# Kernel tuning notes

Hardware: AMD Instinct MI355X
Metric: run time of the kernel (lower is better)

Reference implementation:

```python
import jax, jax.numpy as jnp
import numpy as np
import math

D_MODEL = 1024
N_HEADS = 16
N_QUBITS = 8
HEAD_DIM = D_MODEL // N_HEADS
B, L = 2, 2048


def setup_inputs() -> dict:
    key = jax.random.key(0)
    ks = jax.random.split(key, 16)
    s = 0.02
    return {
        "query": jax.random.normal(ks[0], (B, L, D_MODEL), jnp.float32),
        "key_": jax.random.normal(ks[1], (B, L, D_MODEL), jnp.float32),
        "value": jax.random.normal(ks[2], (B, L, D_MODEL), jnp.float32),
        "Wq": jax.random.normal(ks[3], (D_MODEL, D_MODEL), jnp.float32) * s,
        "bq": jnp.zeros((D_MODEL,), jnp.float32),
        "Wk": jax.random.normal(ks[4], (D_MODEL, D_MODEL), jnp.float32) * s,
        "bk": jnp.zeros((D_MODEL,), jnp.float32),
        "Wv": jax.random.normal(ks[5], (D_MODEL, D_MODEL), jnp.float32) * s,
        "bv": jnp.zeros((D_MODEL,), jnp.float32),
        "Wo": jax.random.normal(ks[6], (D_MODEL, D_MODEL), jnp.float32) * s,
        "bo": jnp.zeros((D_MODEL,), jnp.float32),
        "Wf": jax.random.normal(ks[7], (HEAD_DIM, N_QUBITS), jnp.float32) * s,  # feature map weight (input->qubits)
        "bf": jnp.zeros((N_QUBITS,), jnp.float32),
        "quantum_weights": jax.random.normal(ks[8], (N_HEADS, N_QUBITS), jnp.float32) * 0.1,
        "entanglement_strength": jnp.asarray(0.5, jnp.float32),
    }


def _heads(x):
    # [B, L, D] -> [B, H, L, head_dim]
    b, l, _ = x.shape
    return x.reshape(b, l, N_HEADS, HEAD_DIM).transpose(0, 2, 1, 3)


def reference(query, key_, value, Wq, bq, Wk, bk, Wv, bv, Wo, bo, Wf, bf, quantum_weights, entanglement_strength):
    Qh = _heads(query @ Wq.T + bq)   # [B,H,L,d]
    Kh = _heads(key_ @ Wk.T + bk)
    Vh = _heads(value @ Wv.T + bv)

    classical = jnp.einsum("bhid,bhjd->bhij", Qh, Kh) / math.sqrt(HEAD_DIM)

    # quantum feature map: tanh(linear) -> [B,H,L,Q]
    qq = jnp.tanh(jnp.einsum("bhld,dq->bhlq", Qh, Wf) + bf)
    kq = jnp.tanh(jnp.einsum("bhld,dq->bhlq", Kh, Wf) + bf)

    # mean_q w_q*cos(qq_i - kq_j) == (1/Q)[(w*cos qq)@cos(kq)^T + (w*sin qq)@sin(kq)^T]
    w = jax.nn.sigmoid(quantum_weights)[None, :, None, :]  # [1,H,1,Q]
    quantum = (
        jnp.einsum("bhiq,bhjq->bhij", jnp.cos(qq) * w, jnp.cos(kq))
        + jnp.einsum("bhiq,bhjq->bhij", jnp.sin(qq) * w, jnp.sin(kq))
    ) / N_QUBITS
    ent = jax.nn.sigmoid(entanglement_strength)
    quantum = quantum * ent

    mix = ent  # same sigmoid(entanglement_strength) used as mixing weight
    combined = (1.0 - mix) * classical + mix * quantum

    attn = jax.nn.softmax(combined, axis=-1)  # [B,H,L,L]
    attended = jnp.einsum("bhij,bhjd->bhid", attn, Vh)
    attended = attended.transpose(0, 2, 1, 3).reshape(query.shape[0], query.shape[1], D_MODEL)
    output = attended @ Wo.T + bo
    return output, attn.mean(axis=1)
```

## Files before the change

kernel.cpp:

```cpp
#include <hip/hip_runtime.h>


typedef unsigned short u16;
typedef unsigned int u32;
typedef short v8s __attribute__((ext_vector_type(8)));
typedef float v4f __attribute__((ext_vector_type(4)));

static __device__ __forceinline__ float b2f(u16 h) {
  union { u32 u; float f; } a; a.u = ((u32)h) << 16; return a.f;
}
static __device__ __forceinline__ u16 f2b(float f) {
  union { float f; u32 u; } a; a.f = f;
  u32 u = a.u;
  u32 r = u + 0x7FFFu + ((u >> 16) & 1u);
  return (u16)(r >> 16);
}
static __device__ __forceinline__ u32 fbits(float f) {
  union { float f; u32 u; } a; a.f = f; return a.u;
}
static __device__ __forceinline__ v4f mfma16(v8s a, v8s b, v4f c) {
  return __builtin_amdgcn_mfma_f32_16x16x32_bf16(a, b, c, 0, 0, 0);
}
static __device__ __forceinline__ void gload16(const u16* g, u16* l) {
  __builtin_amdgcn_global_load_lds((const __attribute__((address_space(1))) u32*)g,
                                   (__attribute__((address_space(3))) u32*)l, 16, 0, 0);
}

__global__ __launch_bounds__(256) void k_f2b_all(const float* __restrict__ q, const float* __restrict__ k,
                                                 const float* __restrict__ v, const float* __restrict__ wq,
                                                 const float* __restrict__ wk, const float* __restrict__ wv,
                                                 const float* __restrict__ wo, u16* __restrict__ y) {
  int i = blockIdx.x * 256 + threadIdx.x;
  const float* src; int off;
  if (i < 1048576)      { src = q;  off = i; }
  else if (i < 2097152) { src = k;  off = i - 1048576; }
  else if (i < 3145728) { src = v;  off = i - 2097152; }
  else if (i < 3407872) { src = wq; off = i - 3145728; }
  else if (i < 3670016) { src = wk; off = i - 3407872; }
  else if (i < 3932160) { src = wv; off = i - 3670016; }
  else                  { src = wo; off = i - 3932160; }
  float4 val = ((const float4*)src)[off];
  union { u16 s[4]; uint2 u; } o;
  o.s[0] = f2b(val.x); o.s[1] = f2b(val.y); o.s[2] = f2b(val.z); o.s[3] = f2b(val.w);
  ((uint2*)y)[i] = o.u;
}

__global__ __launch_bounds__(256) void k_gemm128(
    const u16* __restrict__ A0, const u16* __restrict__ A1, const u16* __restrict__ A2,
    const u16* __restrict__ B0, const u16* __restrict__ B1, const u16* __restrict__ B2,
    const float* __restrict__ bias0, const float* __restrict__ bias1, const float* __restrict__ bias2,
    u16* __restrict__ O0, u16* __restrict__ O1, u16* __restrict__ O2t,
    float* __restrict__ Cf) {
  __shared__ __align__(16) u16 pool[18432];
  u16* As = pool;
  u16* Bs = pool + 8192;
  const int K = 1024, N = 1024;
  int t = threadIdx.x, w = t >> 6, lane = t & 63, quad = lane >> 4, l16 = lane & 15;
  int z = blockIdx.z;
  const u16* A = (z == 0) ? A0 : (z == 1) ? A1 : A2;
  const u16* Bm = (z == 0) ? B0 : (z == 1) ? B1 : B2;
  const float* bias = (z == 0) ? bias0 : (z == 1) ? bias1 : bias2;
  int n0 = blockIdx.x * 128, m0 = blockIdx.y * 128;

  int srow = lane >> 2, scol = (lane & 3) * 8;
  const u16* gp[8]; u16* lp[8];
#pragma unroll
  for (int qi = 0; qi < 8; ++qi) {
    int mat = qi >> 2, kk = (qi >> 1) & 1, g = w + (qi & 1) * 4;
    int row = g * 16 + srow;
    gp[qi] = (mat ? Bm + (size_t)(n0 + row) * K : A + (size_t)(m0 + row) * K) + kk * 32 + scol;
    lp[qi] = (mat ? Bs : As) + kk * 4096 + g * 512;
  }

  int mrow = (w >> 1) * 64, ncol = (w & 1) * 64;
  v4f zf = {0.f, 0.f, 0.f, 0.f};
  v4f acc[4][4];
#pragma unroll
  for (int mi = 0; mi < 4; ++mi)
#pragma unroll
    for (int ni = 0; ni < 4; ++ni) acc[mi][ni] = zf;

  for (int k0 = 0; k0 < K; k0 += 64) {
    __syncthreads();
#pragma unroll
    for (int qi = 0; qi < 8; ++qi) gload16(gp[qi] + k0, lp[qi]);
    __syncthreads();
#pragma unroll
    for (int kk = 0; kk < 2; ++kk) {
      v8s af[4], bfr[4];
#pragma unroll
      for (int x = 0; x < 4; ++x) {
        af[x] = *(const v8s*)&As[kk * 4096 + (mrow + x * 16 + l16) * 32 + quad * 8];
        bfr[x] = *(const v8s*)&Bs[kk * 4096 + (ncol + x * 16 + l16) * 32 + quad * 8];
      }
#pragma unroll
      for (int mi = 0; mi < 4; ++mi)
#pragma unroll
        for (int ni = 0; ni < 4; ++ni)
          acc[mi][ni] = mfma16(af[mi], bfr[ni], acc[mi][ni]);
    }
  }

  float bv[4];
#pragma unroll
  for (int ni = 0; ni < 4; ++ni) bv[ni] = bias[n0 + ncol + ni * 16 + l16];

  if (Cf) {
#pragma unroll
    for (int mi = 0; mi < 4; ++mi)
#pragma unroll
      for (int ni = 0; ni < 4; ++ni)
#pragma unroll
        for (int r = 0; r < 4; ++r)
          Cf[(size_t)(m0 + mrow + mi * 16 + quad * 4 + r) * N + n0 + ncol + ni * 16 + l16] =
              acc[mi][ni][r] + bv[ni];
  } else if (z != 2) {
    u16* O = z ? O1 : O0;
#pragma unroll
    for (int mi = 0; mi < 4; ++mi)
#pragma unroll
      for (int ni = 0; ni < 4; ++ni)
#pragma unroll
        for (int r = 0; r < 4; ++r)
          O[(size_t)(m0 + mrow + mi * 16 + quad * 4 + r) * N + n0 + ncol + ni * 16 + l16] =
              f2b(acc[mi][ni][r] + bv[ni]);
  } else {
    __syncthreads();
    u16* Ts = pool + w * 64 * 68;
#pragma unroll
    for (int mi = 0; mi < 4; ++mi)
#pragma unroll
      for (int ni = 0; ni < 4; ++ni)
#pragma unroll
        for (int r = 0; r < 4; ++r)
          Ts[(mi * 16 + quad * 4 + r) * 68 + ni * 16 + l16] = f2b(acc[mi][ni][r] + bv[ni]);
    int c = lane;
    union { uint4 u[8]; u16 s[64]; } cb;
#pragma unroll
    for (int e = 0; e < 64; ++e) cb.s[e] = Ts[e * 68 + c];
    int bb = m0 >> 11, ml = m0 & 2047;
    u16* dst = O2t + ((size_t)(bb * 1024 + n0 + ncol + c)) * 2048 + ml + mrow;
#pragma unroll
    for (int e = 0; e < 8; ++e) *(uint4*)(dst + e * 8) = cb.u[e];
  }
}

__global__ __launch_bounds__(256) void k_features(const u16* __restrict__ Qp, const u16* __restrict__ Kp,
                                                  const float* __restrict__ Wf, const float* __restrict__ bff,
                                                  const float* __restrict__ qw, const float* __restrict__ entp,
                                                  u16* __restrict__ Qaa, u16* __restrict__ Kaa) {
  int isK = blockIdx.y;
  const u16* P = isK ? Kp : Qp;
  u16* Out = isK ? Kaa : Qaa;
  int idx = blockIdx.x * 256 + threadIdx.x;
  int b = idx >> 15, h = (idx >> 11) & 15, l = idx & 2047;
  const u16* src = P + ((size_t)(b * 2048 + l)) * 1024 + h * 64;
  u16* dst = Out + (size_t)idx * 96;
  const float4* Wf4 = (const float4*)Wf;

  float x[64];
#pragma unroll
  for (int g = 0; g < 8; ++g) {
    union { uint4 u; u16 s[8]; } uu;
    uu.u = *(const uint4*)(src + g * 8);
#pragma unroll
    for (int e = 0; e < 8; ++e) x[g * 8 + e] = b2f(uu.s[e]);
  }
  float qv[8];
#pragma unroll
  for (int qq = 0; qq < 8; ++qq) qv[qq] = bff[qq];
#pragma unroll
  for (int d = 0; d < 64; ++d) {
    float4 wa = Wf4[d * 2], wb = Wf4[d * 2 + 1];
    float xd = x[d];
    qv[0] += xd * wa.x; qv[1] += xd * wa.y; qv[2] += xd * wa.z; qv[3] += xd * wa.w;
    qv[4] += xd * wb.x; qv[5] += xd * wb.y; qv[6] += xd * wb.z; qv[7] += xd * wb.w;
  }
  float cs[8], sn[8];
#pragma unroll
  for (int qq = 0; qq < 8; ++qq) {
    float e2 = __expf(2.f * qv[qq]);
    float th = 1.f - 2.f / (e2 + 1.f);
    __sincosf(th, &sn[qq], &cs[qq]);
  }
  float ent = 1.f / (1.f + __expf(-entp[0]));
  union { uint4 u; u16 s[8]; } pc, ps;
  if (!isK) {
#pragma unroll
    for (int g = 0; g < 8; ++g) *(uint4*)(dst + g * 8) = *(const uint4*)(src + g * 8);
#pragma unroll
    for (int qq = 0; qq < 8; ++qq) {
      float sw = 1.f / (1.f + __expf(-qw[h * 8 + qq]));
      pc.s[qq] = f2b(cs[qq] * sw);
      ps.s[qq] = f2b(sn[qq] * sw);
    }
  } else {
    float c1 = (1.f - ent) * 0.125f, c2 = ent * ent * 0.125f;
#pragma unroll
    for (int g = 0; g < 8; ++g) {
      union { uint4 u; u16 s[8]; } ob;
#pragma unroll
      for (int e = 0; e < 8; ++e) ob.s[e] = f2b(x[g * 8 + e] * c1);
      *(uint4*)(dst + g * 8) = ob.u;
    }
#pragma unroll
    for (int qq = 0; qq < 8; ++qq) {
      pc.s[qq] = f2b(cs[qq] * c2);
      ps.s[qq] = f2b(sn[qq] * c2);
    }
  }
  *(uint4*)(dst + 64) = pc.u;
  *(uint4*)(dst + 72) = ps.u;
  uint4 z4 = {0, 0, 0, 0};
  *(uint4*)(dst + 80) = z4;
  *(uint4*)(dst + 88) = z4;
}

__global__ __launch_bounds__(256) void k_flash(const u16* __restrict__ Qa, const u16* __restrict__ Ka,
                                               const u16* __restrict__ VtG, u16* __restrict__ At,
                                               float* __restrict__ lb) {
  __shared__ __align__(16) u16 Ks[2][64][104];
  __shared__ __align__(16) u16 Ps[4][2][16][72];

  int t = threadIdx.x, w = t >> 6, lane = t & 63, quad = lane >> 4, l16 = lane & 15;
  int i0 = blockIdx.x * 128, h = blockIdx.y, b = blockIdx.z;
  size_t qbase = ((size_t)(b * 16 + h)) * 2048 * 96;
  v8s aq[2][3];
#pragma unroll
  for (int i16 = 0; i16 < 2; ++i16) {
    const u16* Qrow = Qa + qbase + (size_t)(i0 + w * 32 + i16 * 16 + l16) * 96;
#pragma unroll
    for (int ks = 0; ks < 3; ++ks) aq[i16][ks] = *(const v8s*)(Qrow + ks * 32 + quad * 8);
  }
  const u16* Kbase = Ka + qbase;
  const u16* Vbase = VtG + ((size_t)(b * 1024 + h * 64)) * 2048;

  const u16* kg[3]; int kdo[3];
#pragma unroll
  for (int p = 0; p < 3; ++p) {
    int idx = t + p * 256, r_ = idx / 12, c_ = idx % 12;
    kg[p] = Kbase + (size_t)r_ * 96 + c_ * 8;
    kdo[p] = r_ * 104 + c_ * 8;
  }
  u16* ks0 = &Ks[0][0][0];
  u16* ks1 = &Ks[1][0][0];

  v4f zf = {0.f, 0.f, 0.f, 0.f};
  v4f oacc[2][4];
#pragma unroll
  for (int i16 = 0; i16 < 2; ++i16)
#pragma unroll
    for (int d16 = 0; d16 < 4; ++d16) oacc[i16][d16] = zf;
  float l_acc[2] = {0.f, 0.f};

  uint4 fk0 = *(const uint4*)kg[0];
  uint4 fk1 = *(const uint4*)kg[1];
  uint4 fk2 = *(const uint4*)kg[2];
  kg[0] += 6144; kg[1] += 6144; kg[2] += 6144;
  *(uint4*)(ks0 + kdo[0]) = fk0;
  *(uint4*)(ks0 + kdo[1]) = fk1;
  *(uint4*)(ks0 + kdo[2]) = fk2;
  fk0 = *(const uint4*)kg[0];
  fk1 = *(const uint4*)kg[1];
  fk2 = *(const uint4*)kg[2];
  kg[0] += 6144; kg[1] += 6144; kg[2] += 6144;
  v8s vf[8];
#pragma unroll
  for (int idx = 0; idx < 8; ++idx)
    vf[idx] = *(const v8s*)(Vbase + (size_t)((idx >> 1) * 16 + l16) * 2048 + (idx & 1) * 32 + quad * 8);
  __syncthreads();

  for (int j0 = 0; j0 < 2048; j0 += 64) {
    int cur = (j0 >> 6) & 1;
    const u16* kb = cur ? ks1 : ks0;
    u16* kw = cur ? ks0 : ks1;
    bool more = (j0 + 64) < 2048;
    if (more) {
      *(uint4*)(kw + kdo[0]) = fk0;
      *(uint4*)(kw + kdo[1]) = fk1;
      *(uint4*)(kw + kdo[2]) = fk2;
    }
    if (j0 + 128 < 2048) {
      fk0 = *(const uint4*)kg[0];
      fk1 = *(const uint4*)kg[1];
      fk2 = *(const uint4*)kg[2];
      kg[0] += 6144; kg[1] += 6144; kg[2] += 6144;
    }
    v8s vn[8];
    if (more) {
#pragma unroll
      for (int idx = 0; idx < 8; ++idx)
        vn[idx] = *(const v8s*)(Vbase + (size_t)((idx >> 1) * 16 + l16) * 2048 + j0 + 64 +
                                (idx & 1) * 32 + quad * 8);
    }

    v4f sacc[2][4];
#pragma unroll
    for (int i16 = 0; i16 < 2; ++i16)
#pragma unroll
      for (int j16 = 0; j16 < 4; ++j16) sacc[i16][j16] = zf;
#pragma unroll
    for (int j16 = 0; j16 < 4; ++j16)
#pragma unroll
      for (int ks = 0; ks < 3; ++ks) {
        v8s kf = *(const v8s*)(kb + (j16 * 16 + l16) * 104 + ks * 32 + quad * 8);
        sacc[0][j16] = mfma16(kf, aq[0][ks], sacc[0][j16]);
        sacc[1][j16] = mfma16(kf, aq[1][ks], sacc[1][j16]);
      }

#pragma unroll
    for (int i16 = 0; i16 < 2; ++i16)
#pragma unroll
      for (int j16 = 0; j16 < 4; ++j16) {
        float e0 = __expf(sacc[i16][j16][0]);
        float e1 = __expf(sacc[i16][j16][1]);
        float e2 = __expf(sacc[i16][j16][2]);
        float e3 = __expf(sacc[i16][j16][3]);
        l_acc[i16] += (e0 + e1) + (e2 + e3);
        uint2 pp;
        pp.x = __builtin_amdgcn_perm(fbits(e1) + 0x8000u, fbits(e0) + 0x8000u, 0x07060302u);
        pp.y = __builtin_amdgcn_perm(fbits(e3) + 0x8000u, fbits(e2) + 0x8000u, 0x07060302u);
        *(uint2*)&Ps[w][i16][l16][j16 * 16 + quad * 4] = pp;
      }
#pragma unroll
    for (int jh = 0; jh < 2; ++jh) {
      v8s pf0 = *(const v8s*)&Ps[w][0][l16][jh * 32 + quad * 8];
      v8s pf1 = *(const v8s*)&Ps[w][1][l16][jh * 32 + quad * 8];
#pragma unroll
      for (int d16 = 0; d16 < 4; ++d16) {
        v8s vv = vf[d16 * 2 + jh];
        oacc[0][d16] = mfma16(pf0, vv, oacc[0][d16]);
        oacc[1][d16] = mfma16(pf1, vv, oacc[1][d16]);
      }
    }
    if (more) {
#pragma unroll
      for (int idx = 0; idx < 8; ++idx) vf[idx] = vn[idx];
      __syncthreads();
    }
  }

#pragma unroll
  for (int i16 = 0; i16 < 2; ++i16) {
    l_acc[i16] += __shfl_xor(l_acc[i16], 16, 64);
    l_acc[i16] += __shfl_xor(l_acc[i16], 32, 64);
    float linv = 1.f / l_acc[i16];
#pragma unroll
    for (int r = 0; r < 4; ++r) {
      float li = __shfl(linv, quad * 4 + r, 64);
      int ri = i0 + w * 32 + i16 * 16 + quad * 4 + r;
#pragma unroll
      for (int d16 = 0; d16 < 4; ++d16)
        At[((size_t)(b * 2048 + ri)) * 1024 + h * 64 + d16 * 16 + l16] = f2b(oacc[i16][d16][r] * li);
    }
    if (lane < 16) {
      size_t mbase = ((size_t)(b * 16 + h)) * 2048;
      lb[mbase + i0 + w * 32 + i16 * 16 + lane] = l_acc[i16];
    }
  }
}

__global__ __launch_bounds__(256) void k_pass2(const u16* __restrict__ Qa, const u16* __restrict__ Ka,
                                               const float* __restrict__ lb,
                                               float* __restrict__ out1) {
  __shared__ __align__(16) u16 Ks[64][104];
  __shared__ float Ls[16][128];
  int t = threadIdx.x, w = t >> 6, lane = t & 63, quad = lane >> 4, l16 = lane & 15;
  int j0 = blockIdx.x * 64, i0 = blockIdx.y * 128, b = blockIdx.z;

#pragma unroll
  for (int rep = 0; rep < 8; ++rep) {
    int idx = t + rep * 256;
    int hh = idx >> 7, il = idx & 127;
    Ls[hh][il] = 0.0625f / lb[((size_t)(b * 16 + hh)) * 2048 + i0 + il];
  }

  size_t base0 = (size_t)b * 16 * 2048 * 96;
  const u16* kg[3]; u16* kd[3];
#pragma unroll
  for (int rep = 0; rep < 3; ++rep) {
    int idx = t + rep * 256;
    int r_ = idx / 12, c_ = idx % 12;
    kg[rep] = Ka + base0 + (size_t)(j0 + r_) * 96 + c_ * 8;
    kd[rep] = &Ks[r_][c_ * 8];
  }
  uint4 f0 = *(const uint4*)kg[0];
  uint4 f1 = *(const uint4*)kg[1];
  uint4 f2 = *(const uint4*)kg[2];

  const u16* q0 = Qa + base0 + (size_t)(i0 + w * 32 + l16) * 96 + quad * 8;
  const u16* q1 = q0 + 16 * 96;

  v4f zf = {0.f, 0.f, 0.f, 0.f};
  v4f macc[2][4];
#pragma unroll
  for (int i16 = 0; i16 < 2; ++i16)
#pragma unroll
    for (int j16 = 0; j16 < 4; ++j16) macc[i16][j16] = zf;

  v8s a[2][3];
#pragma unroll
  for (int ks = 0; ks < 3; ++ks) {
    a[0][ks] = *(const v8s*)(q0 + ks * 32);
    a[1][ks] = *(const v8s*)(q1 + ks * 32);
  }

  for (int h = 0; h < 16; ++h) {
    *(uint4*)kd[0] = f0;
    *(uint4*)kd[1] = f1;
    *(uint4*)kd[2] = f2;
    __syncthreads();
    if (h < 15) {
      kg[0] += 196608; kg[1] += 196608; kg[2] += 196608;
      f0 = *(const uint4*)kg[0];
      f1 = *(const uint4*)kg[1];
      f2 = *(const uint4*)kg[2];
    }

    v4f sacc[2][4];
#pragma unroll
    for (int i16 = 0; i16 < 2; ++i16)
#pragma unroll
      for (int j16 = 0; j16 < 4; ++j16) sacc[i16][j16] = zf;
#pragma unroll
    for (int ks = 0; ks < 3; ++ks)
#pragma unroll
      for (int j16 = 0; j16 < 4; ++j16) {
        v8s kf = *(const v8s*)&Ks[j16 * 16 + l16][ks * 32 + quad * 8];
        sacc[0][j16] = mfma16(a[0][ks], kf, sacc[0][j16]);
        sacc[1][j16] = mfma16(a[1][ks], kf, sacc[1][j16]);
      }

    if (h < 15) {
      q0 += 196608; q1 += 196608;
#pragma unroll
      for (int ks = 0; ks < 3; ++ks) {
        a[0][ks] = *(const v8s*)(q0 + ks * 32);
        a[1][ks] = *(const v8s*)(q1 + ks * 32);
      }
    }

    float li[2][4];
#pragma unroll
    for (int i16 = 0; i16 < 2; ++i16)
#pragma unroll
      for (int r = 0; r < 4; ++r)
        li[i16][r] = Ls[h][w * 32 + i16 * 16 + quad * 4 + r];
#pragma unroll
    for (int i16 = 0; i16 < 2; ++i16)
#pragma unroll
      for (int j16 = 0; j16 < 4; ++j16)
#pragma unroll
        for (int r = 0; r < 4; ++r)
          macc[i16][j16][r] += __expf(sacc[i16][j16][r]) * li[i16][r];
    __syncthreads();
  }

  float* o = out1 + (size_t)b * 2048 * 2048;
#pragma unroll
  for (int i16 = 0; i16 < 2; ++i16)
#pragma unroll
    for (int j16 = 0; j16 < 4; ++j16)
#pragma unroll
      for (int r = 0; r < 4; ++r)
        o[(size_t)(i0 + w * 32 + i16 * 16 + quad * 4 + r) * 2048 + j0 + j16 * 16 + l16] =
            macc[i16][j16][r];
}

extern "C" void kernel_launch(void* const* d_in, const int* in_sizes, int n_in,
                              void* d_out, int out_size, void* d_ws, size_t ws_size,
                              hipStream_t stream) {
  (void)in_sizes; (void)n_in; (void)out_size; (void)ws_size;
  const float* query = (const float*)d_in[0];
  const float* key_  = (const float*)d_in[1];
  const float* value = (const float*)d_in[2];
  const float* Wq = (const float*)d_in[3];
  const float* bq = (const float*)d_in[4];
  const float* Wk = (const float*)d_in[5];
  const float* bk = (const float*)d_in[6];
  const float* Wv = (const float*)d_in[7];
  const float* bv = (const float*)d_in[8];
  const float* Wo = (const float*)d_in[9];
  const float* bo = (const float*)d_in[10];
  const float* Wf = (const float*)d_in[11];
  const float* bff = (const float*)d_in[12];
  const float* qw = (const float*)d_in[13];
  const float* entp = (const float*)d_in[14];

  char* p = (char*)d_ws;
  u16* Xq  = (u16*)(p + 0);
  u16* Xk  = (u16*)(p + 8388608);
  u16* Xv  = (u16*)(p + 16777216);
  u16* Wqb = (u16*)(p + 25165824);
  u16* Wkb = (u16*)(p + 27262976);
  u16* Wvb = (u16*)(p + 29360128);
  u16* Qp  = (u16*)(p + 33554432);
  u16* Kp  = (u16*)(p + 41943040);
  u16* VtG = (u16*)(p + 50331648);
  u16* Qaa = (u16*)(p + 58720256);
  u16* Kaa = (u16*)(p + 71303168);
  float* lb = (float*)(p + 84148224);
  u16* At  = (u16*)(p + 84410368);
  u16* Wob = (u16*)(p + 31457280);

  k_f2b_all<<<16384, 256, 0, stream>>>(query, key_, value, Wq, Wk, Wv, Wo, Xq);

  k_gemm128<<<dim3(8, 32, 3), 256, 0, stream>>>(Xq, Xk, Xv, Wqb, Wkb, Wvb, bq, bk, bv,
                                                Qp, Kp, VtG, nullptr);

  k_features<<<dim3(256, 2), 256, 0, stream>>>(Qp, Kp, Wf, bff, qw, entp, Qaa, Kaa);

  k_flash<<<dim3(16, 16, 2), 256, 0, stream>>>(Qaa, Kaa, VtG, At, lb);

  k_pass2<<<dim3(32, 16, 2), 256, 0, stream>>>(Qaa, Kaa, lb, (float*)d_out + 4194304);

  k_gemm128<<<dim3(8, 32, 1), 256, 0, stream>>>(At, At, At, Wob, Wob, Wob, bo, bo, bo,
                                                nullptr, nullptr, nullptr, (float*)d_out);
}
```

Baseline: 350.5 us.

## Restructure flash kernel: smaller query tiles, async K loads to LDS, exp2 and packed bf16

The flash kernel now covers 64 query rows per block instead of 128, so the grid doubles and occupancy rises (launch bounds 256,4). K tiles are copied straight into LDS with global_load_lds double buffering instead of staging through registers, and V is loaded directly each iteration. LOG2E is folded into the K scaling so both the flash and pass2 kernels can use the raw v_exp_f32 (exp2) instruction, and P is packed to bf16 with v_cvt_pk_bf16_f32. s_setprio hints are placed around the MFMA phases. The trade-off is that K and V are loaded from global memory twice as often overall, and V loads are no longer prefetched.

```diff
diff --git a/kernel.cpp b/kernel.cpp
--- a/kernel.cpp
+++ b/kernel.cpp
@@ -15,15 +15,18 @@
   u32 r = u + 0x7FFFu + ((u >> 16) & 1u);
   return (u16)(r >> 16);
 }
-static __device__ __forceinline__ u32 fbits(float f) {
-  union { float f; u32 u; } a; a.f = f; return a.u;
-}
 static __device__ __forceinline__ v4f mfma16(v8s a, v8s b, v4f c) {
   return __builtin_amdgcn_mfma_f32_16x16x32_bf16(a, b, c, 0, 0, 0);
 }
 static __device__ __forceinline__ void gload16(const u16* g, u16* l) {
   __builtin_amdgcn_global_load_lds((const __attribute__((address_space(1))) u32*)g,
                                    (__attribute__((address_space(3))) u32*)l, 16, 0, 0);
+}
+static __device__ __forceinline__ float exp2fast(float x) {
+  float r; asm("v_exp_f32 %0, %1" : "=v"(r) : "v"(x)); return r;
+}
+static __device__ __forceinline__ u32 cvtpk_bf16(float lo, float hi) {
+  u32 r; asm("v_cvt_pk_bf16_f32 %0, %1, %2" : "=v"(r) : "v"(lo), "v"(hi)); return r;
 }
 
 __global__ __launch_bounds__(256) void k_f2b_all(const float* __restrict__ q, const float* __restrict__ k,
@@ -195,7 +198,8 @@
       ps.s[qq] = f2b(sn[qq] * sw);
     }
   } else {
-    float c1 = (1.f - ent) * 0.125f, c2 = ent * ent * 0.125f;
+    const float LOG2E = 1.44269504088896f;
+    float c1 = (1.f - ent) * 0.125f * LOG2E, c2 = ent * ent * 0.125f * LOG2E;
 #pragma unroll
     for (int g = 0; g < 8; ++g) {
       union { uint4 u; u16 s[8]; } ob;
@@ -216,147 +220,104 @@
   *(uint4*)(dst + 88) = z4;
 }
 
-__global__ __launch_bounds__(256) void k_flash(const u16* __restrict__ Qa, const u16* __restrict__ Ka,
-                                               const u16* __restrict__ VtG, u16* __restrict__ At,
-                                               float* __restrict__ lb) {
-  __shared__ __align__(16) u16 Ks[2][64][104];
-  __shared__ __align__(16) u16 Ps[4][2][16][72];
+__global__ __launch_bounds__(256, 4) void k_flash(const u16* __restrict__ Qa, const u16* __restrict__ Ka,
+                                                  const u16* __restrict__ VtG, u16* __restrict__ At,
+                                                  float* __restrict__ lb) {
+  __shared__ __align__(16) u16 Ks[2][6144];
+  __shared__ __align__(16) u16 Ps[4][16][72];
 
   int t = threadIdx.x, w = t >> 6, lane = t & 63, quad = lane >> 4, l16 = lane & 15;
-  int i0 = blockIdx.x * 128, h = blockIdx.y, b = blockIdx.z;
+  int i0 = blockIdx.x * 64, h = blockIdx.y, b = blockIdx.z;
   size_t qbase = ((size_t)(b * 16 + h)) * 2048 * 96;
-  v8s aq[2][3];
-#pragma unroll
-  for (int i16 = 0; i16 < 2; ++i16) {
-    const u16* Qrow = Qa + qbase + (size_t)(i0 + w * 32 + i16 * 16 + l16) * 96;
-#pragma unroll
-    for (int ks = 0; ks < 3; ++ks) aq[i16][ks] = *(const v8s*)(Qrow + ks * 32 + quad * 8);
-  }
   const u16* Kbase = Ka + qbase;
   const u16* Vbase = VtG + ((size_t)(b * 1024 + h * 64)) * 2048;
 
-  const u16* kg[3]; int kdo[3];
-#pragma unroll
-  for (int p = 0; p < 3; ++p) {
-    int idx = t + p * 256, r_ = idx / 12, c_ = idx % 12;
-    kg[p] = Kbase + (size_t)r_ * 96 + c_ * 8;
-    kdo[p] = r_ * 104 + c_ * 8;
-  }
-  u16* ks0 = &Ks[0][0][0];
-  u16* ks1 = &Ks[1][0][0];
+  int goff = w * 512 + lane * 8;
+  int loff = w * 512;
+
+#pragma unroll
+  for (int p = 0; p < 3; ++p)
+    gload16(Kbase + p * 2048 + goff, &Ks[0][p * 2048 + loff]);
+
+  v8s aq[3];
+  {
+    const u16* Qrow = Qa + qbase + (size_t)(i0 + w * 16 + l16) * 96;
+#pragma unroll
+    for (int ks = 0; ks < 3; ++ks) aq[ks] = *(const v8s*)(Qrow + ks * 32 + quad * 8);
+  }
 
   v4f zf = {0.f, 0.f, 0.f, 0.f};
-  v4f oacc[2][4];
-#pragma unroll
-  for (int i16 = 0; i16 < 2; ++i16)
-#pragma unroll
-    for (int d16 = 0; d16 < 4; ++d16) oacc[i16][d16] = zf;
-  float l_acc[2] = {0.f, 0.f};
-
-  uint4 fk0 = *(const uint4*)kg[0];
-  uint4 fk1 = *(const uint4*)kg[1];
-  uint4 fk2 = *(const uint4*)kg[2];
-  kg[0] += 6144; kg[1] += 6144; kg[2] += 6144;
-  *(uint4*)(ks0 + kdo[0]) = fk0;
-  *(uint4*)(ks0 + kdo[1]) = fk1;
-  *(uint4*)(ks0 + kdo[2]) = fk2;
-  fk0 = *(const uint4*)kg[0];
-  fk1 = *(const uint4*)kg[1];
-  fk2 = *(const uint4*)kg[2];
-  kg[0] += 6144; kg[1] += 6144; kg[2] += 6144;
-  v8s vf[8];
-#pragma unroll
-  for (int idx = 0; idx < 8; ++idx)
-    vf[idx] = *(const v8s*)(Vbase + (size_t)((idx >> 1) * 16 + l16) * 2048 + (idx & 1) * 32 + quad * 8);
+  v4f oacc[4] = {zf, zf, zf, zf};
+  float l_acc = 0.f;
+
   __syncthreads();
 
   for (int j0 = 0; j0 < 2048; j0 += 64) {
     int cur = (j0 >> 6) & 1;
-    const u16* kb = cur ? ks1 : ks0;
-    u16* kw = cur ? ks0 : ks1;
-    bool more = (j0 + 64) < 2048;
-    if (more) {
-      *(uint4*)(kw + kdo[0]) = fk0;
-      *(uint4*)(kw + kdo[1]) = fk1;
-      *(uint4*)(kw + kdo[2]) = fk2;
-    }
-    if (j0 + 128 < 2048) {
-      fk0 = *(const uint4*)kg[0];
-      fk1 = *(const uint4*)kg[1];
-      fk2 = *(const uint4*)kg[2];
-      kg[0] += 6144; kg[1] += 6144; kg[2] += 6144;
-    }
-    v8s vn[8];
-    if (more) {
-#pragma unroll
-      for (int idx = 0; idx < 8; ++idx)
-        vn[idx] = *(const v8s*)(Vbase + (size_t)((idx >> 1) * 16 + l16) * 2048 + j0 + 64 +
-                                (idx & 1) * 32 + quad * 8);
-    }
-
-    v4f sacc[2][4];
-#pragma unroll
-    for (int i16 = 0; i16 < 2; ++i16)
-#pragma unroll
-      for (int j16 = 0; j16 < 4; ++j16) sacc[i16][j16] = zf;
+    const u16* kb = Ks[cur];
+
+    v8s vf[8];
+#pragma unroll
+    for (int idx = 0; idx < 8; ++idx)
+      vf[idx] = *(const v8s*)(Vbase + (size_t)((idx >> 1) * 16 + l16) * 2048 + j0 +
+                              (idx & 1) * 32 + quad * 8);
+    if (j0 + 64 < 2048) {
+      const u16* src = Kbase + (size_t)(j0 + 64) * 96;
+#pragma unroll
+      for (int p = 0; p < 3; ++p)
+        gload16(src + p * 2048 + goff, &Ks[cur ^ 1][p * 2048 + loff]);
+    }
+
+    v4f sacc[4] = {zf, zf, zf, zf};
+    __builtin_amdgcn_s_setprio(1);
 #pragma unroll
     for (int j16 = 0; j16 < 4; ++j16)
 #pragma unroll
       for (int ks = 0; ks < 3; ++ks) {
-        v8s kf = *(const v8s*)(kb + (j16 * 16 + l16) * 104 + ks * 32 + quad * 8);
-        sacc[0][j16] = mfma16(kf, aq[0][ks], sacc[0][j16]);
-        sacc[1][j16] = mfma16(kf, aq[1][ks], sacc[1][j16]);
+        v8s kf = *(const v8s*)(kb + (j16 * 16 + l16) * 96 + ks * 32 + quad * 8);
+        sacc[j16] = mfma16(kf, aq[ks], sacc[j16]);
       }
-
-#pragma unroll
-    for (int i16 = 0; i16 < 2; ++i16)
-#pragma unroll
-      for (int j16 = 0; j16 < 4; ++j16) {
-        float e0 = __expf(sacc[i16][j16][0]);
-        float e1 = __expf(sacc[i16][j16][1]);
-        float e2 = __expf(sacc[i16][j16][2]);
-        float e3 = __expf(sacc[i16][j16][3]);
-        l_acc[i16] += (e0 + e1) + (e2 + e3);
-        uint2 pp;
-        pp.x = __builtin_amdgcn_perm(fbits(e1) + 0x8000u, fbits(e0) + 0x8000u, 0x07060302u);
-        pp.y = __builtin_amdgcn_perm(fbits(e3) + 0x8000u, fbits(e2) + 0x8000u, 0x07060302u);
-        *(uint2*)&Ps[w][i16][l16][j16 * 16 + quad * 4] = pp;
-      }
+    __builtin_amdgcn_s_setprio(0);
+
+#pragma unroll
+    for (int j16 = 0; j16 < 4; ++j16) {
+      float e0 = exp2fast(sacc[j16][0]);
+      float e1 = exp2fast(sacc[j16][1]);
+      float e2 = exp2fast(sacc[j16][2]);
+      float e3 = exp2fast(sacc[j16][3]);
+      l_acc += (e0 + e1) + (e2 + e3);
+      uint2 pp;
+      pp.x = cvtpk_bf16(e0, e1);
+      pp.y = cvtpk_bf16(e2, e3);
+      *(uint2*)&Ps[w][l16][j16 * 16 + quad * 4] = pp;
+    }
+
+    __builtin_amdgcn_s_setprio(1);
 #pragma unroll
     for (int jh = 0; jh < 2; ++jh) {
-      v8s pf0 = *(const v8s*)&Ps[w][0][l16][jh * 32 + quad * 8];
-      v8s pf1 = *(const v8s*)&Ps[w][1][l16][jh * 32 + quad * 8];
-#pragma unroll
-      for (int d16 = 0; d16 < 4; ++d16) {
-        v8s vv = vf[d16 * 2 + jh];
-        oacc[0][d16] = mfma16(pf0, vv, oacc[0][d16]);
-        oacc[1][d16] = mfma16(pf1, vv, oacc[1][d16]);
-      }
-    }
-    if (more) {
-#pragma unroll
-      for (int idx = 0; idx < 8; ++idx) vf[idx] = vn[idx];
-      __syncthreads();
-    }
-  }
-
-#pragma unroll
-  for (int i16 = 0; i16 < 2; ++i16) {
-    l_acc[i16] += __shfl_xor(l_acc[i16], 16, 64);
-    l_acc[i16] += __shfl_xor(l_acc[i16], 32, 64);
-    float linv = 1.f / l_acc[i16];
-#pragma unroll
-    for (int r = 0; r < 4; ++r) {
-      float li = __shfl(linv, quad * 4 + r, 64);
-      int ri = i0 + w * 32 + i16 * 16 + quad * 4 + r;
+      v8s pf = *(const v8s*)&Ps[w][l16][jh * 32 + quad * 8];
 #pragma unroll
       for (int d16 = 0; d16 < 4; ++d16)
-        At[((size_t)(b * 2048 + ri)) * 1024 + h * 64 + d16 * 16 + l16] = f2b(oacc[i16][d16][r] * li);
-    }
-    if (lane < 16) {
-      size_t mbase = ((size_t)(b * 16 + h)) * 2048;
-      lb[mbase + i0 + w * 32 + i16 * 16 + lane] = l_acc[i16];
-    }
+        oacc[d16] = mfma16(pf, vf[d16 * 2 + jh], oacc[d16]);
+    }
+    __builtin_amdgcn_s_setprio(0);
+    __syncthreads();
+  }
+
+  l_acc += __shfl_xor(l_acc, 16, 64);
+  l_acc += __shfl_xor(l_acc, 32, 64);
+  float linv = 1.f / l_acc;
+#pragma unroll
+  for (int r = 0; r < 4; ++r) {
+    float li = __shfl(linv, quad * 4 + r, 64);
+    int ri = i0 + w * 16 + quad * 4 + r;
+#pragma unroll
+    for (int d16 = 0; d16 < 4; ++d16)
+      At[((size_t)(b * 2048 + ri)) * 1024 + h * 64 + d16 * 16 + l16] = f2b(oacc[d16][r] * li);
+  }
+  if (lane < 16) {
+    size_t mbase = ((size_t)(b * 16 + h)) * 2048;
+    lb[mbase + i0 + w * 16 + lane] = l_acc;
   }
 }
 
@@ -452,7 +413,7 @@
       for (int j16 = 0; j16 < 4; ++j16)
 #pragma unroll
         for (int r = 0; r < 4; ++r)
-          macc[i16][j16][r] += __expf(sacc[i16][j16][r]) * li[i16][r];
+          macc[i16][j16][r] += exp2fast(sacc[i16][j16][r]) * li[i16][r];
     __syncthreads();
   }
 
@@ -510,7 +471,7 @@
 
   k_features<<<dim3(256, 2), 256, 0, stream>>>(Qp, Kp, Wf, bff, qw, entp, Qaa, Kaa);
 
-  k_flash<<<dim3(16, 16, 2), 256, 0, stream>>>(Qaa, Kaa, VtG, At, lb);
+  k_flash<<<dim3(32, 16, 2), 256, 0, stream>>>(Qaa, Kaa, VtG, At, lb);
 
   k_pass2<<<dim3(32, 16, 2), 256, 0, stream>>>(Qaa, Kaa, lb, (float*)d_out + 4194304);
 
```

After: 392.7 us. +12.0%, slower.
